# Kernel tuning notes

Measured on AMD Instinct MI355X. Metric: run time of the kernel, lower is better.

The kernel has to match this reference:

```python
import math
import jax, jax.numpy as jnp
import numpy as np


def setup_inputs() -> dict:
    key = jax.random.key(0)
    T, C = 8192, 2048
    layer_depth, num_layers = 5, 10
    ks = jax.random.split(key, 8)

    x = jax.random.normal(ks[0], (T, C), jnp.float32)
    sx = jax.random.normal(ks[1], (C,), jnp.float32)
    aa = jnp.zeros((C,), jnp.float32)
    bb = jnp.zeros((C,), jnp.float32)
    pp = jnp.zeros((C,), jnp.float32)

    # parameter initial values per TimeMix.setup
    r01 = layer_depth / (num_layers - 1)
    r10 = 1.0 - layer_depth / num_layers
    zigzag = 0.5 * (jnp.arange(1, C + 1) % 3 - 1).astype(jnp.float32)
    time_first = jnp.full((C,), math.log(0.3), jnp.float32) + zigzag
    h = jnp.arange(C, dtype=jnp.float32)
    time_decay = (-5.0 + 8.0 * (h / (C - 1)) ** (0.7 + 1.3 * r01)).astype(jnp.float32)
    xr = jnp.arange(C, dtype=jnp.float32) / C
    time_mix_k = xr ** r10
    time_mix_v = time_mix_k + 0.3 * r01
    time_mix_r = xr ** (0.5 * r10)

    ln_scale = jnp.ones((C,), jnp.float32)
    ln_bias = jnp.zeros((C,), jnp.float32)

    s = 1.0 / np.sqrt(C)  # lecun-normal-ish scale for Dense kernels
    Wk = jax.random.normal(ks[2], (C, C), jnp.float32) * s
    Wv = jax.random.normal(ks[3], (C, C), jnp.float32) * s
    Wr = jax.random.normal(ks[4], (C, C), jnp.float32) * s
    Wo = jax.random.normal(ks[5], (C, C), jnp.float32) * s

    return dict(x=x, sx=sx, aa=aa, bb=bb, pp=pp,
                time_first=time_first, time_decay=time_decay,
                time_mix_k=time_mix_k, time_mix_v=time_mix_v, time_mix_r=time_mix_r,
                ln_scale=ln_scale, ln_bias=ln_bias,
                Wk=Wk, Wv=Wv, Wr=Wr, Wo=Wo)


def reference(x, sx, aa, bb, pp, time_first, time_decay,
              time_mix_k, time_mix_v, time_mix_r,
              ln_scale, ln_bias, Wk, Wv, Wr, Wo):
    # LayerNorm(eps=1e-5)
    mu = jnp.mean(x, axis=-1, keepdims=True)
    var = jnp.var(x, axis=-1, keepdims=True)
    xx = (x - mu) * jax.lax.rsqrt(var + 1e-5) * ln_scale + ln_bias  # [T, C]

    # token shift: previous timestep (sx state for t=0)
    sxs = jnp.concatenate((sx[None, :], xx[:-1, :]), axis=0)  # [T, C]
    kx = xx * time_mix_k + sxs * (1.0 - time_mix_k)
    vx = xx * time_mix_v + sxs * (1.0 - time_mix_v)
    rx = xx * time_mix_r + sxs * (1.0 - time_mix_r)

    r = jax.nn.sigmoid(rx @ Wr)  # [T, C]
    k = kx @ Wk                  # [T, C]
    v = vx @ Wv                  # [T, C]

    w = -jnp.exp(time_decay)     # [C]

    def step(state, kv):
        aa, bb, pp = state
        kk, vv = kv
        # output with numerically-stable log-sum-exp style bookkeeping
        ww = time_first + kk
        p = jnp.maximum(pp, ww)
        e1 = jnp.exp(pp - p)
        e2 = jnp.exp(ww - p)
        out = ((e1 * aa + e2 * vv) / (e1 * bb + e2)).astype(r.dtype)
        # state update
        ww2 = w + pp
        p2 = jnp.maximum(ww2, kk)
        e1b = jnp.exp(ww2 - p2)
        e2b = jnp.exp(kk - p2)
        aa = e1b * aa + e2b * vv
        bb = e1b * bb + e2b
        return (aa, bb, p2), out

    (aa, bb, pp), wkv = jax.lax.scan(step, (aa, bb, pp), (k, v))  # wkv: [T, C]

    out = x + (r * wkv) @ Wo
    return (out, xx[-1, :], aa, bb, pp)
```

## Files before the change

kernel.cpp:

```cpp
#include <hip/hip_runtime.h>
#include <stdint.h>

#define T_DIM 8192
#define C_DIM 2048
#define LCHUNK 128
#define NCHUNK (T_DIM / LCHUNK)

typedef unsigned short u16;
typedef __bf16 bf16x8_t __attribute__((ext_vector_type(8)));
typedef float f32x4_t __attribute__((ext_vector_type(4)));

__device__ __forceinline__ u16 f2bf(float f) {
    union { float f; uint32_t u; } x; x.f = f;
    uint32_t r = x.u + 0x7fffu + ((x.u >> 16) & 1u);
    return (u16)(r >> 16);
}
__device__ __forceinline__ float bf2f(u16 u) {
    union { uint32_t u; float f; } x; x.u = ((uint32_t)u) << 16;
    return x.f;
}
__device__ __forceinline__ void gload16(const void* g, void* l) {
    __builtin_amdgcn_global_load_lds((const __attribute__((address_space(1))) uint32_t*)g,
                                     (__attribute__((address_space(3))) uint32_t*)l, 16, 0, 0);
}
__device__ __forceinline__ f32x4_t mfma16(bf16x8_t a, bf16x8_t b, f32x4_t c) {
    return __builtin_amdgcn_mfma_f32_16x16x32_bf16(a, b, c, 0, 0, 0);
}

__global__ __launch_bounds__(256)
void transpose_cast(const float* __restrict__ W0, const float* __restrict__ W1,
                    const float* __restrict__ W2, const float* __restrict__ W3,
                    u16* __restrict__ Wt)
{
    __shared__ float tile[32][33];
    const int z = blockIdx.z;
    const float* W = (z == 0) ? W0 : (z == 1) ? W1 : (z == 2) ? W2 : W3;
    u16* Tm = Wt + (size_t)z * C_DIM * C_DIM;
    const int tx = threadIdx.x & 31, ty = threadIdx.x >> 5;
    const int bn = blockIdx.x * 32, bk = blockIdx.y * 32;
#pragma unroll
    for (int i = 0; i < 4; ++i)
        tile[ty + 8 * i][tx] = W[(size_t)(bk + ty + 8 * i) * C_DIM + bn + tx];
    __syncthreads();
#pragma unroll
    for (int i = 0; i < 4; ++i)
        Tm[(size_t)(bn + ty + 8 * i) * C_DIM + bk + tx] = f2bf(tile[tx][ty + 8 * i]);
}

union F8 { float4 v[2]; float f[8]; };

__global__ __launch_bounds__(256)
void ln_mix_kernel(const float* __restrict__ x, const float* __restrict__ sx,
                   const float* __restrict__ lns, const float* __restrict__ lnb,
                   const float* __restrict__ tmk, const float* __restrict__ tmv,
                   const float* __restrict__ tmr,
                   u16* __restrict__ kx, u16* __restrict__ vx, u16* __restrict__ rx,
                   float* __restrict__ xx_last)
{
    const int t = blockIdx.x;
    const int tid = threadIdx.x;
    const size_t rowoff = (size_t)t * C_DIM;

    F8 a, p;
    const float4* xt = (const float4*)(x + rowoff);
    a.v[0] = xt[2 * tid]; a.v[1] = xt[2 * tid + 1];
    const float4* xp = (t == 0) ? (const float4*)sx : (const float4*)(x + rowoff - C_DIM);
    p.v[0] = xp[2 * tid]; p.v[1] = xp[2 * tid + 1];

    float s1 = 0.f, s2 = 0.f, s3 = 0.f, s4 = 0.f;
#pragma unroll
    for (int i = 0; i < 8; ++i) {
        s1 += a.f[i]; s2 += a.f[i] * a.f[i];
        s3 += p.f[i]; s4 += p.f[i] * p.f[i];
    }
#pragma unroll
    for (int off = 32; off; off >>= 1) {
        s1 += __shfl_down(s1, off);
        s2 += __shfl_down(s2, off);
        s3 += __shfl_down(s3, off);
        s4 += __shfl_down(s4, off);
    }
    __shared__ float red[4][4];
    if ((tid & 63) == 0) {
        red[0][tid >> 6] = s1; red[1][tid >> 6] = s2;
        red[2][tid >> 6] = s3; red[3][tid >> 6] = s4;
    }
    __syncthreads();
    s1 = red[0][0] + red[0][1] + red[0][2] + red[0][3];
    s2 = red[1][0] + red[1][1] + red[1][2] + red[1][3];
    s3 = red[2][0] + red[2][1] + red[2][2] + red[2][3];
    s4 = red[3][0] + red[3][1] + red[3][2] + red[3][3];
    const float inv = 1.0f / (float)C_DIM;
    const float mu = s1 * inv;
    const float rstd = rsqrtf(s2 * inv - mu * mu + 1e-5f);
    const float mup = s3 * inv;
    const float rstdp = rsqrtf(s4 * inv - mup * mup + 1e-5f);

    F8 ls, lb, mk, mv, mr;
    { const float4* q = (const float4*)lns; ls.v[0] = q[2*tid]; ls.v[1] = q[2*tid+1]; }
    { const float4* q = (const float4*)lnb; lb.v[0] = q[2*tid]; lb.v[1] = q[2*tid+1]; }
    { const float4* q = (const float4*)tmk; mk.v[0] = q[2*tid]; mk.v[1] = q[2*tid+1]; }
    { const float4* q = (const float4*)tmv; mv.v[0] = q[2*tid]; mv.v[1] = q[2*tid+1]; }
    { const float4* q = (const float4*)tmr; mr.v[0] = q[2*tid]; mr.v[1] = q[2*tid+1]; }

    union { u16 u[8]; uint4 q; } ok, ov, orr;
#pragma unroll
    for (int i = 0; i < 8; ++i) {
        const float xxv  = (a.f[i] - mu) * rstd * ls.f[i] + lb.f[i];
        const float prev = (t == 0) ? p.f[i] : (p.f[i] - mup) * rstdp * ls.f[i] + lb.f[i];
        ok.u[i]  = f2bf(xxv * mk.f[i] + prev * (1.f - mk.f[i]));
        ov.u[i]  = f2bf(xxv * mv.f[i] + prev * (1.f - mv.f[i]));
        orr.u[i] = f2bf(xxv * mr.f[i] + prev * (1.f - mr.f[i]));
        if (t == T_DIM - 1) xx_last[tid * 8 + i] = xxv;
    }
    ((uint4*)(kx + rowoff))[tid] = ok.q;
    ((uint4*)(vx + rowoff))[tid] = ov.q;
    ((uint4*)(rx + rowoff))[tid] = orr.q;
}

__device__ __forceinline__ void gemm_core(
    const u16* __restrict__ A, const u16* __restrict__ Bt,
    void* __restrict__ Cout, const float* __restrict__ resid,
    const int mode, const int N, const int K,
    const int m0, const int n0, u16* lds)
{
    const int tid = threadIdx.x;
    const int wave = tid >> 6, lane = tid & 63;
    const int wm = wave >> 1, wn = wave & 1;
    const int fr = lane & 15, fo = lane >> 4;
    const int sw = (fo ^ ((fr >> 1) & 3)) * 8;

    f32x4_t acc[4][4] = {};

    const int lrow = lane >> 2;
    const int scol = ((lane & 3) ^ ((lane >> 3) & 3)) * 8;
    const u16* gA = A  + (size_t)(m0 + wave * 16 + lrow) * K + scol;
    const u16* gB = Bt + (size_t)(n0 + wave * 16 + lrow) * K + scol;
    const size_t rk64 = (size_t)64 * K;
    const int dA = wave * 512;
    const int dB = 4096 + wave * 512;

    auto stage = [&](int t) {
        const int b = (t & 1) * 8192;
        const u16* ga = gA + (size_t)t * 32;
        const u16* gb = gB + (size_t)t * 32;
        gload16(ga,        lds + b + dA);
        gload16(ga + rk64, lds + b + dA + 2048);
        gload16(gb,        lds + b + dB);
        gload16(gb + rk64, lds + b + dB + 2048);
    };

    const int NT = K >> 5;
    stage(0);
    asm volatile("s_waitcnt vmcnt(0)" ::: "memory");
    asm volatile("s_barrier" ::: "memory");

    for (int t = 0; t < NT; ++t) {
        if (t + 1 < NT) stage(t + 1);
        const u16* lA = lds + (t & 1) * 8192 + (wm * 64 + fr) * 32;
        const u16* lB = lds + (t & 1) * 8192 + 4096 + (wn * 64 + fr) * 32;
        bf16x8_t a[4], b[4];
#pragma unroll
        for (int i = 0; i < 4; ++i) {
            a[i] = *(const bf16x8_t*)(lA + i * 512 + sw);
            b[i] = *(const bf16x8_t*)(lB + i * 512 + sw);
        }
        __builtin_amdgcn_s_setprio(1);
#pragma unroll
        for (int mi = 0; mi < 4; ++mi)
#pragma unroll
            for (int ni = 0; ni < 4; ++ni)
                acc[mi][ni] = mfma16(a[mi], b[ni], acc[mi][ni]);
        __builtin_amdgcn_s_setprio(0);
        asm volatile("s_waitcnt vmcnt(0)" ::: "memory");
        asm volatile("s_barrier" ::: "memory");
    }

    const int r4 = fo * 4;
#pragma unroll
    for (int mi = 0; mi < 4; ++mi) {
#pragma unroll
        for (int ni = 0; ni < 4; ++ni) {
            const int col = n0 + wn * 64 + ni * 16 + fr;
#pragma unroll
            for (int i = 0; i < 4; ++i) {
                const int row = m0 + wm * 64 + mi * 16 + r4 + i;
                float v = acc[mi][ni][i];
                if (resid) v += resid[(size_t)row * N + col];
                if (mode == 0)      ((float*)Cout)[(size_t)row * N + col] = v;
                else if (mode == 1) ((u16*)Cout)[(size_t)row * N + col] = f2bf(v);
                else {
                    const float s = 1.f / (1.f + __expf(-v));
                    ((u16*)Cout)[(size_t)row * N + col] = f2bf(s);
                }
            }
        }
    }
}

__global__ __launch_bounds__(256, 4)
void gemm_kvr(const u16* __restrict__ kx, const u16* __restrict__ vx, const u16* __restrict__ rxp,
              const u16* __restrict__ Wt,
              u16* __restrict__ kbuf, u16* __restrict__ vbuf, u16* __restrict__ rbuf)
{
    __shared__ u16 lds[16384];
    const int which = blockIdx.y;
    const int m0 = (int)(blockIdx.x & 63) << 7;
    const int n0 = (int)(blockIdx.x >> 6) << 7;
    const u16* A = (which == 0) ? kx : (which == 1) ? vx : rxp;
    const u16* B = Wt + (size_t)which * C_DIM * C_DIM;
    u16* C = (which == 0) ? kbuf : (which == 1) ? vbuf : rbuf;
    gemm_core(A, B, C, nullptr, (which == 2) ? 2 : 1, C_DIM, C_DIM, m0, n0, lds);
}

__global__ __launch_bounds__(256, 4)
void gemm_o(const u16* __restrict__ Aw, const u16* __restrict__ Wt3,
            float* __restrict__ out, const float* __restrict__ x)
{
    __shared__ u16 lds[16384];
    const int m0 = (int)(blockIdx.x & 63) << 7;
    const int n0 = (int)(blockIdx.x >> 6) << 7;
    gemm_core(Aw, Wt3, out, x, 0, C_DIM, C_DIM, m0, n0, lds);
}

__global__ __launch_bounds__(256)
void scan_partial(const u16* __restrict__ k, const u16* __restrict__ v,
                  const float* __restrict__ time_decay,
                  float* __restrict__ pA, float* __restrict__ pB, float* __restrict__ pP)
{
    const int c = blockIdx.y * 256 + threadIdx.x;
    const int j = blockIdx.x;
    const float w = -__expf(time_decay[c]);
    float aa = 0.f, bb = 0.f, pp = -1e30f;
    const u16* kp = k + (size_t)j * LCHUNK * C_DIM + c;
    const u16* vp = v + (size_t)j * LCHUNK * C_DIM + c;
#pragma unroll 4
    for (int i = 0; i < LCHUNK; ++i) {
        const float kk = bf2f(*kp);
        const float vv = bf2f(*vp);
        kp += C_DIM; vp += C_DIM;
        const float ww = w + pp;
        const float p2 = fmaxf(ww, kk);
        const float e1 = __expf(ww - p2);
        const float e2 = __expf(kk - p2);
        aa = e1 * aa + e2 * vv;
        bb = e1 * bb + e2;
        pp = p2;
    }
    const int o = j * C_DIM + c;
    pA[o] = aa; pB[o] = bb; pP[o] = pp;
}

__global__ __launch_bounds__(256)
void scan_combine(const float* __restrict__ pA, const float* __restrict__ pB,
                  const float* __restrict__ pP,
                  const float* __restrict__ aa_in, const float* __restrict__ bb_in,
                  const float* __restrict__ pp_in,
                  const float* __restrict__ time_decay,
                  float* __restrict__ sA, float* __restrict__ sB, float* __restrict__ sP)
{
    const int c = blockIdx.x * 256 + threadIdx.x;
    const float wL = -__expf(time_decay[c]) * (float)LCHUNK;
    float a = aa_in[c], b = bb_in[c], p = pp_in[c];
    for (int j = 0; j < NCHUNK; ++j) {
        const int o = j * C_DIM + c;
        sA[o] = a; sB[o] = b; sP[o] = p;
        const float A = pA[o], B = pB[o], P = pP[o];
        const float pd = p + wL;
        const float q = fmaxf(pd, P);
        const float e1 = __expf(pd - q), e2 = __expf(P - q);
        a = e1 * a + e2 * A;
        b = e1 * b + e2 * B;
        p = q;
    }
}

__global__ __launch_bounds__(256)
void scan_out(const u16* __restrict__ k, const u16* __restrict__ v,
              const u16* __restrict__ r,
              const float* __restrict__ time_decay, const float* __restrict__ time_first,
              const float* __restrict__ sA, const float* __restrict__ sB,
              const float* __restrict__ sP,
              u16* __restrict__ arwkv,
              float* __restrict__ aa_out, float* __restrict__ bb_out, float* __restrict__ pp_out)
{
    const int c = blockIdx.y * 256 + threadIdx.x;
    const int j = blockIdx.x;
    const float w = -__expf(time_decay[c]);
    const float u = time_first[c];
    const int so = j * C_DIM + c;
    float aa = sA[so], bb = sB[so], pp = sP[so];
    const size_t base = (size_t)j * LCHUNK * C_DIM + c;
    const u16* kp = k + base;
    const u16* vp = v + base;
    const u16* rp = r + base;
    u16* op = arwkv + base;
#pragma unroll 4
    for (int i = 0; i < LCHUNK; ++i) {
        const float kk = bf2f(*kp);
        const float vv = bf2f(*vp);
        const float sr = bf2f(*rp);
        kp += C_DIM; vp += C_DIM; rp += C_DIM;
        const float ww = u + kk;
        const float p = fmaxf(pp, ww);
        const float e1 = __expf(pp - p);
        const float e2 = __expf(ww - p);
        const float out = (e1 * aa + e2 * vv) / (e1 * bb + e2);
        *op = f2bf(sr * out);
        op += C_DIM;
        const float ww2 = w + pp;
        const float p2 = fmaxf(ww2, kk);
        const float f1 = __expf(ww2 - p2);
        const float f2 = __expf(kk - p2);
        aa = f1 * aa + f2 * vv;
        bb = f1 * bb + f2;
        pp = p2;
    }
    if (j == NCHUNK - 1) { aa_out[c] = aa; bb_out[c] = bb; pp_out[c] = pp; }
}

extern "C" void kernel_launch(void* const* d_in, const int* in_sizes, int n_in,
                              void* d_out, int out_size, void* d_ws, size_t ws_size,
                              hipStream_t stream)
{
    (void)in_sizes; (void)n_in; (void)out_size; (void)ws_size;
    const float* x          = (const float*)d_in[0];
    const float* sx         = (const float*)d_in[1];
    const float* aa_in      = (const float*)d_in[2];
    const float* bb_in      = (const float*)d_in[3];
    const float* pp_in      = (const float*)d_in[4];
    const float* time_first = (const float*)d_in[5];
    const float* time_decay = (const float*)d_in[6];
    const float* tmk        = (const float*)d_in[7];
    const float* tmv        = (const float*)d_in[8];
    const float* tmr        = (const float*)d_in[9];
    const float* lns        = (const float*)d_in[10];
    const float* lnb        = (const float*)d_in[11];
    const float* Wk         = (const float*)d_in[12];
    const float* Wv         = (const float*)d_in[13];
    const float* Wr         = (const float*)d_in[14];
    const float* Wo         = (const float*)d_in[15];

    float* out     = (float*)d_out;
    float* xx_last = out + (size_t)T_DIM * C_DIM;
    float* aa_out  = xx_last + C_DIM;
    float* bb_out  = aa_out + C_DIM;
    float* pp_out  = bb_out + C_DIM;

    const size_t TC = (size_t)T_DIM * C_DIM;
    const size_t C2 = (size_t)C_DIM * C_DIM;
    u16* kx    = (u16*)d_ws;
    u16* vx    = kx + TC;
    u16* rx    = vx + TC;
    u16* Wt    = rx + TC;
    u16* kbuf  = Wt + 4 * C2;
    u16* vbuf  = kbuf + TC;
    u16* rbuf  = vbuf + TC;
    float* pA  = (float*)(rbuf + TC);
    float* pB  = pA + (size_t)NCHUNK * C_DIM;
    float* pP  = pB + (size_t)NCHUNK * C_DIM;
    float* sA  = pP + (size_t)NCHUNK * C_DIM;
    float* sB  = sA + (size_t)NCHUNK * C_DIM;
    float* sP  = sB + (size_t)NCHUNK * C_DIM;
    u16* arwkv = rx;

    transpose_cast<<<dim3(C_DIM / 32, C_DIM / 32, 4), 256, 0, stream>>>(Wk, Wv, Wr, Wo, Wt);
    ln_mix_kernel<<<T_DIM, 256, 0, stream>>>(x, sx, lns, lnb, tmk, tmv, tmr, kx, vx, rx, xx_last);

    const int NB = (T_DIM / 128) * (C_DIM / 128);
    gemm_kvr<<<dim3(NB, 3), 256, 0, stream>>>(kx, vx, rx, Wt, kbuf, vbuf, rbuf);

    scan_partial<<<dim3(NCHUNK, C_DIM / 256), 256, 0, stream>>>(kbuf, vbuf, time_decay, pA, pB, pP);
    scan_combine<<<C_DIM / 256, 256, 0, stream>>>(pA, pB, pP, aa_in, bb_in, pp_in, time_decay, sA, sB, sP);
    scan_out<<<dim3(NCHUNK, C_DIM / 256), 256, 0, stream>>>(kbuf, vbuf, rbuf, time_decay, time_first,
                                                            sA, sB, sP, arwkv, aa_out, bb_out, pp_out);

    gemm_o<<<NB, 256, 0, stream>>>(arwkv, Wt + 3 * C2, out, x);
}
```

Before: 484.7 us.

## Merge prep kernels and overlap r-projection GEMM with chunk scan partials

Weight transpose/cast and layernorm-mix run as one combined launch, with the block index selecting which job a block does. The r-projection GEMM is split out of the k/v GEMM launch and placed in the same launch as the scan_partial blocks. The memory-bound scan partials can then run alongside compute-bound GEMM tiles. This removes launch gaps and tail idle time, but the larger shared-memory footprint of the merged prep kernel may lower occupancy for its layernorm blocks.

```diff
diff --git a/kernel.cpp b/kernel.cpp
--- a/kernel.cpp
+++ b/kernel.cpp
@@ -27,38 +27,41 @@
     return __builtin_amdgcn_mfma_f32_16x16x32_bf16(a, b, c, 0, 0, 0);
 }
 
+union F8 { float4 v[2]; float f[8]; };
+
 __global__ __launch_bounds__(256)
-void transpose_cast(const float* __restrict__ W0, const float* __restrict__ W1,
-                    const float* __restrict__ W2, const float* __restrict__ W3,
-                    u16* __restrict__ Wt)
-{
-    __shared__ float tile[32][33];
-    const int z = blockIdx.z;
-    const float* W = (z == 0) ? W0 : (z == 1) ? W1 : (z == 2) ? W2 : W3;
-    u16* Tm = Wt + (size_t)z * C_DIM * C_DIM;
-    const int tx = threadIdx.x & 31, ty = threadIdx.x >> 5;
-    const int bn = blockIdx.x * 32, bk = blockIdx.y * 32;
-#pragma unroll
-    for (int i = 0; i < 4; ++i)
-        tile[ty + 8 * i][tx] = W[(size_t)(bk + ty + 8 * i) * C_DIM + bn + tx];
-    __syncthreads();
-#pragma unroll
-    for (int i = 0; i < 4; ++i)
-        Tm[(size_t)(bn + ty + 8 * i) * C_DIM + bk + tx] = f2bf(tile[tx][ty + 8 * i]);
-}
-
-union F8 { float4 v[2]; float f[8]; };
-
-__global__ __launch_bounds__(256)
-void ln_mix_kernel(const float* __restrict__ x, const float* __restrict__ sx,
-                   const float* __restrict__ lns, const float* __restrict__ lnb,
-                   const float* __restrict__ tmk, const float* __restrict__ tmv,
-                   const float* __restrict__ tmr,
-                   u16* __restrict__ kx, u16* __restrict__ vx, u16* __restrict__ rx,
-                   float* __restrict__ xx_last)
-{
-    const int t = blockIdx.x;
+void prep_kernel(const float* __restrict__ W0, const float* __restrict__ W1,
+                 const float* __restrict__ W2, const float* __restrict__ W3,
+                 u16* __restrict__ Wt,
+                 const float* __restrict__ x, const float* __restrict__ sx,
+                 const float* __restrict__ lns, const float* __restrict__ lnb,
+                 const float* __restrict__ tmk, const float* __restrict__ tmv,
+                 const float* __restrict__ tmr,
+                 u16* __restrict__ kx, u16* __restrict__ vx, u16* __restrict__ rx,
+                 float* __restrict__ xx_last)
+{
+    __shared__ float shf[32 * 33];
+    const int bid = blockIdx.x;
     const int tid = threadIdx.x;
+
+    if (bid < 16384) {
+        const int z = bid >> 12;
+        const int rem = bid & 4095;
+        const int bn = (rem & 63) * 32, bk = (rem >> 6) * 32;
+        const float* W = (z == 0) ? W0 : (z == 1) ? W1 : (z == 2) ? W2 : W3;
+        u16* Tm = Wt + (size_t)z * C_DIM * C_DIM;
+        const int tx = tid & 31, ty = tid >> 5;
+#pragma unroll
+        for (int i = 0; i < 4; ++i)
+            shf[(ty + 8 * i) * 33 + tx] = W[(size_t)(bk + ty + 8 * i) * C_DIM + bn + tx];
+        __syncthreads();
+#pragma unroll
+        for (int i = 0; i < 4; ++i)
+            Tm[(size_t)(bn + ty + 8 * i) * C_DIM + bk + tx] = f2bf(shf[tx * 33 + ty + 8 * i]);
+        return;
+    }
+
+    const int t = bid - 16384;
     const size_t rowoff = (size_t)t * C_DIM;
 
     F8 a, p;
@@ -80,16 +83,16 @@
         s3 += __shfl_down(s3, off);
         s4 += __shfl_down(s4, off);
     }
-    __shared__ float red[4][4];
+    float* red = shf;
     if ((tid & 63) == 0) {
-        red[0][tid >> 6] = s1; red[1][tid >> 6] = s2;
-        red[2][tid >> 6] = s3; red[3][tid >> 6] = s4;
+        red[0 * 4 + (tid >> 6)] = s1; red[1 * 4 + (tid >> 6)] = s2;
+        red[2 * 4 + (tid >> 6)] = s3; red[3 * 4 + (tid >> 6)] = s4;
     }
     __syncthreads();
-    s1 = red[0][0] + red[0][1] + red[0][2] + red[0][3];
-    s2 = red[1][0] + red[1][1] + red[1][2] + red[1][3];
-    s3 = red[2][0] + red[2][1] + red[2][2] + red[2][3];
-    s4 = red[3][0] + red[3][1] + red[3][2] + red[3][3];
+    s1 = red[0] + red[1] + red[2] + red[3];
+    s2 = red[4] + red[5] + red[6] + red[7];
+    s3 = red[8] + red[9] + red[10] + red[11];
+    s4 = red[12] + red[13] + red[14] + red[15];
     const float inv = 1.0f / (float)C_DIM;
     const float mu = s1 * inv;
     const float rstd = rsqrtf(s2 * inv - mu * mu + 1e-5f);
@@ -199,41 +202,42 @@
 }
 
 __global__ __launch_bounds__(256, 4)
-void gemm_kvr(const u16* __restrict__ kx, const u16* __restrict__ vx, const u16* __restrict__ rxp,
-              const u16* __restrict__ Wt,
-              u16* __restrict__ kbuf, u16* __restrict__ vbuf, u16* __restrict__ rbuf)
+void gemm_kv(const u16* __restrict__ kx, const u16* __restrict__ vx,
+             const u16* __restrict__ Wt,
+             u16* __restrict__ kbuf, u16* __restrict__ vbuf)
 {
     __shared__ u16 lds[16384];
     const int which = blockIdx.y;
     const int m0 = (int)(blockIdx.x & 63) << 7;
     const int n0 = (int)(blockIdx.x >> 6) << 7;
-    const u16* A = (which == 0) ? kx : (which == 1) ? vx : rxp;
+    const u16* A = (which == 0) ? kx : vx;
     const u16* B = Wt + (size_t)which * C_DIM * C_DIM;
-    u16* C = (which == 0) ? kbuf : (which == 1) ? vbuf : rbuf;
-    gemm_core(A, B, C, nullptr, (which == 2) ? 2 : 1, C_DIM, C_DIM, m0, n0, lds);
+    u16* C = (which == 0) ? kbuf : vbuf;
+    gemm_core(A, B, C, nullptr, 1, C_DIM, C_DIM, m0, n0, lds);
 }
 
 __global__ __launch_bounds__(256, 4)
-void gemm_o(const u16* __restrict__ Aw, const u16* __restrict__ Wt3,
-            float* __restrict__ out, const float* __restrict__ x)
+void gemm_r_partial(const u16* __restrict__ rxp, const u16* __restrict__ Wt2,
+                    u16* __restrict__ rbuf,
+                    const u16* __restrict__ kbuf, const u16* __restrict__ vbuf,
+                    const float* __restrict__ time_decay,
+                    float* __restrict__ pA, float* __restrict__ pB, float* __restrict__ pP)
 {
     __shared__ u16 lds[16384];
-    const int m0 = (int)(blockIdx.x & 63) << 7;
-    const int n0 = (int)(blockIdx.x >> 6) << 7;
-    gemm_core(Aw, Wt3, out, x, 0, C_DIM, C_DIM, m0, n0, lds);
-}
-
-__global__ __launch_bounds__(256)
-void scan_partial(const u16* __restrict__ k, const u16* __restrict__ v,
-                  const float* __restrict__ time_decay,
-                  float* __restrict__ pA, float* __restrict__ pB, float* __restrict__ pP)
-{
-    const int c = blockIdx.y * 256 + threadIdx.x;
-    const int j = blockIdx.x;
+    const int bid = blockIdx.x;
+    if (bid < 1024) {
+        const int m0 = (bid & 63) << 7;
+        const int n0 = (bid >> 6) << 7;
+        gemm_core(rxp, Wt2, rbuf, nullptr, 2, C_DIM, C_DIM, m0, n0, lds);
+        return;
+    }
+    const int sb = bid - 1024;
+    const int j = sb & 63;
+    const int c = (sb >> 6) * 256 + threadIdx.x;
     const float w = -__expf(time_decay[c]);
     float aa = 0.f, bb = 0.f, pp = -1e30f;
-    const u16* kp = k + (size_t)j * LCHUNK * C_DIM + c;
-    const u16* vp = v + (size_t)j * LCHUNK * C_DIM + c;
+    const u16* kp = kbuf + (size_t)j * LCHUNK * C_DIM + c;
+    const u16* vp = vbuf + (size_t)j * LCHUNK * C_DIM + c;
 #pragma unroll 4
     for (int i = 0; i < LCHUNK; ++i) {
         const float kk = bf2f(*kp);
@@ -319,6 +323,16 @@
     if (j == NCHUNK - 1) { aa_out[c] = aa; bb_out[c] = bb; pp_out[c] = pp; }
 }
 
+__global__ __launch_bounds__(256, 4)
+void gemm_o(const u16* __restrict__ Aw, const u16* __restrict__ Wt3,
+            float* __restrict__ out, const float* __restrict__ x)
+{
+    __shared__ u16 lds[16384];
+    const int m0 = (int)(blockIdx.x & 63) << 7;
+    const int n0 = (int)(blockIdx.x >> 6) << 7;
+    gemm_core(Aw, Wt3, out, x, 0, C_DIM, C_DIM, m0, n0, lds);
+}
+
 extern "C" void kernel_launch(void* const* d_in, const int* in_sizes, int n_in,
                               void* d_out, int out_size, void* d_ws, size_t ws_size,
                               hipStream_t stream)
@@ -364,16 +378,16 @@
     float* sP  = sB + (size_t)NCHUNK * C_DIM;
     u16* arwkv = rx;
 
-    transpose_cast<<<dim3(C_DIM / 32, C_DIM / 32, 4), 256, 0, stream>>>(Wk, Wv, Wr, Wo, Wt);
-    ln_mix_kernel<<<T_DIM, 256, 0, stream>>>(x, sx, lns, lnb, tmk, tmv, tmr, kx, vx, rx, xx_last);
+    prep_kernel<<<16384 + T_DIM, 256, 0, stream>>>(Wk, Wv, Wr, Wo, Wt,
+                                                   x, sx, lns, lnb, tmk, tmv, tmr,
+                                                   kx, vx, rx, xx_last);
 
     const int NB = (T_DIM / 128) * (C_DIM / 128);
-    gemm_kvr<<<dim3(NB, 3), 256, 0, stream>>>(kx, vx, rx, Wt, kbuf, vbuf, rbuf);
-
-    scan_partial<<<dim3(NCHUNK, C_DIM / 256), 256, 0, stream>>>(kbuf, vbuf, time_decay, pA, pB, pP);
+    gemm_kv<<<dim3(NB, 2), 256, 0, stream>>>(kx, vx, Wt, kbuf, vbuf);
+    gemm_r_partial<<<NB + NCHUNK * (C_DIM / 256), 256, 0, stream>>>(
+        rx, Wt + 2 * C2, rbuf, kbuf, vbuf, time_decay, pA, pB, pP);
     scan_combine<<<C_DIM / 256, 256, 0, stream>>>(pA, pB, pP, aa_in, bb_in, pp_in, time_decay, sA, sB, sP);
     scan_out<<<dim3(NCHUNK, C_DIM / 256), 256, 0, stream>>>(kbuf, vbuf, rbuf, time_decay, time_first,
                                                             sA, sB, sP, arwkv, aa_out, bb_out, pp_out);
-
     gemm_o<<<NB, 256, 0, stream>>>(arwkv, Wt + 3 * C2, out, x);
 }
```

After: 476.5 us. About the same (-1.7%).
